# Kernel optimization log

Measured on AMD Instinct MI355X. Metric: run time of the kernel, lower is better.

## Reference

```python
import jax, jax.numpy as jnp
import numpy as np

N_E = 1024
E_DIM = 256
BETA = 0.25
PERSISTENCE = 0.1
B, T = 16, 1024


def setup_inputs() -> dict:
    key = jax.random.key(0)
    k1, k2 = jax.random.split(key)
    z = jax.random.normal(k1, (B, T, E_DIM), dtype=jnp.float32)
    # nn.Embedding(1+n_e, e_dim) init uniform(-1/n_e, 1/n_e)
    emb_weight = jax.random.uniform(k2, (N_E + 1, E_DIM), dtype=jnp.float32,
                                    minval=-1.0 / N_E, maxval=1.0 / N_E)
    return {"z": z, "emb_weight": emb_weight}


def _loss_contrast(z, ind, book):
    # z: (B,T,e), ind: (B,T) int, book: (n_e+1, e)
    z_q = book[ind]                                   # (B,T,e)
    loss_indices = jnp.sum((z - z_q) ** 2, axis=-1)   # (B,T)
    # ||z - book||^2 expanded to avoid the (B,T,n_e+1,e) intermediate
    z_sq = jnp.sum(z * z, axis=-1)                    # (B,T)
    b_sq = jnp.sum(book * book, axis=-1)              # (n_e+1,)
    cross = jnp.einsum('bte,ne->btn', z, book)        # (B,T,n_e+1)
    loss_all = z_sq[..., None] + b_sq[None, None, :] - 2.0 * cross
    lc = jnp.maximum(loss_indices[..., None] - loss_all + 1e-6 / N_E, 0.0)
    return jnp.mean(lc)


def _forward(z, emb_weight):
    zf = z.reshape(-1, E_DIM)
    d = (jnp.sum(zf * zf, axis=1, keepdims=True)
         + jnp.sum(emb_weight * emb_weight, axis=1)
         - 2.0 * (zf @ emb_weight.T)).reshape(B, T, N_E + 1)

    ind0 = jnp.clip(jnp.argmin(d[:, 0, :], axis=1), 0, N_E - 1)  # (B,)

    def step(carry, d_t):
        ind, coe = carry                              # (B,) int, (B,) f32
        d_here = jnp.take_along_axis(d_t, ind[:, None], axis=1)[:, 0]
        ind_next = jnp.minimum(ind + 1, N_E - 1)
        d_next = jnp.take_along_axis(d_t, ind_next[:, None], axis=1)[:, 0]
        stay = d_here <= d_next - coe
        ind_new = jnp.where(stay, ind, ind_next)
        coe_new = jnp.where(stay, coe + PERSISTENCE / N_E, 0.0)
        return (ind_new, coe_new), ind_new

    coe0 = jnp.zeros((B,), jnp.float32)
    _, inds = jax.lax.scan(step, (ind0, coe0), jnp.swapaxes(d[:, 1:, :], 0, 1))
    encoding_indices = jnp.concatenate([ind0[None, :], inds], axis=0).T  # (B,T)

    book_sg = jax.lax.stop_gradient(emb_weight)  # torch uses .data/.detach() everywhere
    z_q_raw = book_sg[encoding_indices]
    z_q = z + jax.lax.stop_gradient(z_q_raw - z)  # straight-through

    # non-legacy: beta * L(z, sg(book)) + L(sg(z), sg(book))
    loss = (BETA * _loss_contrast(z, encoding_indices, book_sg)
            + _loss_contrast(jax.lax.stop_gradient(z), encoding_indices, book_sg))

    v = jnp.max(encoding_indices) - jnp.min(encoding_indices)
    return z_q, loss, encoding_indices, v


def reference(z, emb_weight):
    return _forward(z, emb_weight)
```

## Files before the change

kernel.cpp:

```cpp
#include <hip/hip_runtime.h>

#define N_E   1024
#define EDIM  256
#define BB    16
#define TT    1024
#define NROW  (BB*TT)
#define NCOL  1025
#define NPAD  1152
#define PERS  (0.1f/1024.0f)
#define EPSC  (1e-6f/1024.0f)

#define OUT_LOSS 4194304
#define OUT_IDX  4194305
#define OUT_V    4210689

#define WS_ZB   0ull
#define WS_BBF  8388608ull
#define WS_BSQ  8978432ull
#define WS_E    8983552ull
#define WS_IND  84481024ull
#define WS_PART 84546560ull

typedef __attribute__((ext_vector_type(8))) short short8;
typedef __attribute__((ext_vector_type(4))) float floatx4;

__device__ __forceinline__ unsigned short f2bf(float f) {
    unsigned int u = __float_as_uint(f);
    u = (u + 0x7fffu + ((u >> 16) & 1u)) >> 16;
    return (unsigned short)u;
}

__global__ __launch_bounds__(256) void k0_prep(const float* __restrict__ z,
                                               const float* __restrict__ book,
                                               unsigned short* __restrict__ zb,
                                               unsigned short* __restrict__ bb,
                                               float* __restrict__ bsq) {
    int bx = blockIdx.x, tid = threadIdx.x;
    if (bx < 4096) {
        float4 v = ((const float4*)z)[bx * 256 + tid];
        size_t o = ((size_t)bx * 256 + tid) * 4;
        zb[o + 0] = f2bf(v.x); zb[o + 1] = f2bf(v.y);
        zb[o + 2] = f2bf(v.z); zb[o + 3] = f2bf(v.w);
    } else {
        int row = bx - 4096;
        float v = (row < NCOL) ? book[(size_t)row * EDIM + tid] : 0.0f;
        bb[(size_t)row * EDIM + tid] = f2bf(v);
        __shared__ float sd[256];
        sd[tid] = v * v;
        __syncthreads();
        for (int s = 128; s > 0; s >>= 1) { if (tid < s) sd[tid] += sd[tid + s]; __syncthreads(); }
        if (tid == 0) bsq[row] = sd[0];
    }
}

__global__ __launch_bounds__(256) void k1_gemm(const unsigned short* __restrict__ zb,
                                               const unsigned short* __restrict__ bb,
                                               const float* __restrict__ bsq,
                                               float* __restrict__ e) {
    int tid = threadIdx.x;
    int lane = tid & 63, w = tid >> 6;
    int mBase = blockIdx.x * 128 + (w >> 1) * 64;
    int nBase = blockIdx.y * 128 + (w & 1) * 64;
    int r = lane & 15, q = lane >> 4;

    floatx4 acc[4][4];
    #pragma unroll
    for (int i = 0; i < 4; i++)
        #pragma unroll
        for (int j = 0; j < 4; j++) acc[i][j] = (floatx4){0.f, 0.f, 0.f, 0.f};

    const short8* A = (const short8*)zb;
    const short8* Bm = (const short8*)bb;

    #pragma unroll
    for (int ks = 0; ks < 8; ks++) {
        int k8 = ks * 4 + q;
        short8 a[4], b[4];
        #pragma unroll
        for (int i = 0; i < 4; i++) a[i] = A[(size_t)(mBase + i * 16 + r) * 32 + k8];
        #pragma unroll
        for (int j = 0; j < 4; j++) b[j] = Bm[(size_t)(nBase + j * 16 + r) * 32 + k8];
        #pragma unroll
        for (int i = 0; i < 4; i++)
            #pragma unroll
            for (int j = 0; j < 4; j++)
                acc[i][j] = __builtin_amdgcn_mfma_f32_16x16x32_bf16(a[i], b[j], acc[i][j], 0, 0, 0);
    }

    float bsql[4];
    #pragma unroll
    for (int j = 0; j < 4; j++) bsql[j] = bsq[nBase + j * 16 + r];

    #pragma unroll
    for (int i = 0; i < 4; i++)
        #pragma unroll
        for (int rr = 0; rr < 4; rr++) {
            int m = mBase + i * 16 + q * 4 + rr;
            float* erow = e + (size_t)m * NPAD;
            #pragma unroll
            for (int j = 0; j < 4; j++)
                erow[nBase + j * 16 + r] = fmaf(-2.0f, acc[i][j][rr], bsql[j]);
        }
}

__global__ __launch_bounds__(256) void k2_scan(const float* __restrict__ z,
                                               const float* __restrict__ book,
                                               const float* __restrict__ bsq,
                                               const float* __restrict__ e,
                                               int* __restrict__ wind) {
    int b = blockIdx.x, tid = threadIdx.x;
    int lane = tid & 63, w = tid >> 6;

    const float4* zr = (const float4*)(z + (size_t)b * TT * EDIM);
    float4 zv = zr[lane];
    float s = zv.x * zv.x + zv.y * zv.y + zv.z * zv.z + zv.w * zv.w;
    #pragma unroll
    for (int off = 32; off; off >>= 1) s += __shfl_xor(s, off, 64);
    float zsq = s;

    float best = 3.4e38f; int bidx = 0;
    for (int wi = w; wi < 17; wi += 4) {
        int n = wi * 64 + lane;
        if (n < NCOL) {
            const float4* br = (const float4*)(book + (size_t)n * EDIM);
            float c0 = 0.f, c1 = 0.f, c2 = 0.f, c3 = 0.f;
            #pragma unroll 8
            for (int k = 0; k < 64; k++) {
                float4 bo = br[k]; float4 za = zr[k];
                c0 = fmaf(za.x, bo.x, c0); c1 = fmaf(za.y, bo.y, c1);
                c2 = fmaf(za.z, bo.z, c2); c3 = fmaf(za.w, bo.w, c3);
            }
            float cr = (c0 + c1) + (c2 + c3);
            float d0 = (zsq + bsq[n]) - 2.0f * cr;
            if (d0 < best || (d0 == best && n < bidx)) { best = d0; bidx = n; }
        }
    }
    #pragma unroll
    for (int off = 32; off; off >>= 1) {
        float ob = __shfl_xor(best, off, 64);
        int   oi = __shfl_xor(bidx, off, 64);
        if (ob < best || (ob == best && oi < bidx)) { best = ob; bidx = oi; }
    }
    __shared__ float sb[4]; __shared__ int si[4];
    if (lane == 0) { sb[w] = best; si[w] = bidx; }
    __syncthreads();
    if (w != 0) return;

    best = sb[0]; bidx = si[0];
    for (int i = 1; i < 4; i++) {
        float vv = sb[i]; int ii = si[i];
        if (vv < best || (vv == best && ii < bidx)) { best = vv; bidx = ii; }
    }

    int ind = min(bidx, N_E - 1);
    float coe = 0.0f;
    size_t ibase = (size_t)b * TT;
    if (lane == 0) wind[ibase] = ind;

    const float* eb = e + (size_t)b * TT * NPAD;
    float cur[30], nxt[30];
    int cb_cur = min(ind, 960);
    #pragma unroll
    for (int j = 0; j < 30; j++)
        cur[j] = eb[(size_t)(1 + j) * NPAD + cb_cur + lane];

    int t = 1;
    while (t < 1024) {
        int cb_nxt = min(ind, 960);
        #pragma unroll
        for (int j = 0; j < 30; j++) {
            int tn = t + 30 + j; tn = tn < 1024 ? tn : 1023;
            nxt[j] = eb[(size_t)tn * NPAD + cb_nxt + lane];
        }
        int packed = 0;
        #pragma unroll
        for (int j = 0; j < 30; j++) {
            if (t + j < 1024) {
                float here = __uint_as_float(__builtin_amdgcn_readlane(
                                 __float_as_uint(cur[j]), ind - cb_cur));
                int nc = min(ind + 1, N_E - 1);
                float nv = __uint_as_float(__builtin_amdgcn_readlane(
                                 __float_as_uint(cur[j]), nc - cb_cur));
                bool stay = (here <= nv - coe);
                ind = stay ? ind : nc;
                coe = stay ? (coe + PERS) : 0.0f;
                packed = (lane == j) ? ind : packed;
            }
        }
        if (lane < 30 && (t + lane) < 1024) wind[ibase + t + lane] = packed;
        #pragma unroll
        for (int j = 0; j < 30; j++) cur[j] = nxt[j];
        cb_cur = cb_nxt;
        t += 30;
    }
}

__global__ __launch_bounds__(256) void k3_loss_zq(const float* __restrict__ e,
                                                  const int* __restrict__ wind,
                                                  const float* __restrict__ book,
                                                  float* __restrict__ part,
                                                  float* __restrict__ out) {
    int rIdx = blockIdx.x, tid = threadIdx.x;
    int ind = wind[rIdx];
    const float* er = e + (size_t)rIdx * NPAD;
    float eind = er[ind];
    float p = 0.0f;
    for (int n = tid; n < NCOL; n += 256) {
        float v = eind - er[n] + EPSC;
        p += v > 0.0f ? v : 0.0f;
    }
    __shared__ float sd[256];
    sd[tid] = p; __syncthreads();
    for (int s = 128; s > 0; s >>= 1) { if (tid < s) sd[tid] += sd[tid + s]; __syncthreads(); }
    if (tid == 0) { part[rIdx] = sd[0]; out[OUT_IDX + rIdx] = (float)ind; }
    out[(size_t)rIdx * 256 + tid] = book[(size_t)ind * EDIM + tid];
}

__global__ __launch_bounds__(256) void k4_final(const float* __restrict__ part,
                                                const int* __restrict__ wind,
                                                float* __restrict__ out) {
    int tid = threadIdx.x;
    float s = 0.0f;
    for (int i = tid; i < NROW; i += 256) s += part[i];
    __shared__ float sd[256];
    sd[tid] = s; __syncthreads();
    for (int st = 128; st > 0; st >>= 1) { if (tid < st) sd[tid] += sd[tid + st]; __syncthreads(); }
    if (tid == 0) {
        int mn = wind[0], mx = wind[TT - 1];
        for (int b = 1; b < BB; b++) {
            mn = min(mn, wind[(size_t)b * TT]);
            mx = max(mx, wind[(size_t)b * TT + TT - 1]);
        }
        out[OUT_LOSS] = 1.25f * sd[0] / ((float)NROW * (float)NCOL);
        out[OUT_V] = (float)(mx - mn);
    }
}

extern "C" void kernel_launch(void* const* d_in, const int* in_sizes, int n_in,
                              void* d_out, int out_size, void* d_ws, size_t ws_size,
                              hipStream_t stream) {
    const float* z    = (const float*)d_in[0];
    const float* book = (const float*)d_in[1];
    char* ws = (char*)d_ws;
    unsigned short* zb = (unsigned short*)(ws + WS_ZB);
    unsigned short* bb = (unsigned short*)(ws + WS_BBF);
    float* bsq  = (float*)(ws + WS_BSQ);
    float* e    = (float*)(ws + WS_E);
    int*   wind = (int*)(ws + WS_IND);
    float* part = (float*)(ws + WS_PART);
    float* out  = (float*)d_out;

    hipLaunchKernelGGL(k0_prep,    dim3(4096 + 1152), dim3(256), 0, stream, z, book, zb, bb, bsq);
    hipLaunchKernelGGL(k1_gemm,    dim3(128, 9),      dim3(256), 0, stream, zb, bb, bsq, e);
    hipLaunchKernelGGL(k2_scan,    dim3(16),          dim3(256), 0, stream, z, book, bsq, e, wind);
    hipLaunchKernelGGL(k3_loss_zq, dim3(16384),       dim3(256), 0, stream, e, wind, book, part, out);
    hipLaunchKernelGGL(k4_final,   dim3(1),           dim3(256), 0, stream, part, wind, out);
}
```

Baseline: 263.0 us.

## Quantize scan stay-test into integer thresholds with one readlane per step

The sequential per-batch scan now precomputes, for each lane and time step, an integer threshold floor((d_next - d_here)/PERS). This turns the float comparison with the accumulating coe into an integer counter test, so each serial step needs one readlane instead of two and a shorter dependency chain. The chunk size grows from 30 to 31 steps so the loop covers exactly 1023 steps with no bounds checks. The quantization may not exactly match the float comparison in edge cases, since the reference accumulates coe as a float sum.

```diff
diff --git a/kernel.cpp b/kernel.cpp
--- a/kernel.cpp
+++ b/kernel.cpp
@@ -103,11 +103,11 @@
         }
 }
 
-__global__ __launch_bounds__(256) void k2_scan(const float* __restrict__ z,
-                                               const float* __restrict__ book,
-                                               const float* __restrict__ bsq,
-                                               const float* __restrict__ e,
-                                               int* __restrict__ wind) {
+__global__ __launch_bounds__(256, 1) void k2_scan(const float* __restrict__ z,
+                                                  const float* __restrict__ book,
+                                                  const float* __restrict__ bsq,
+                                                  const float* __restrict__ e,
+                                                  int* __restrict__ wind) {
     int b = blockIdx.x, tid = threadIdx.x;
     int lane = tid & 63, w = tid >> 6;
 
@@ -153,45 +153,64 @@
     }
 
     int ind = min(bidx, N_E - 1);
-    float coe = 0.0f;
+    int kk = 0;
     size_t ibase = (size_t)b * TT;
     if (lane == 0) wind[ibase] = ind;
 
     const float* eb = e + (size_t)b * TT * NPAD;
-    float cur[30], nxt[30];
-    int cb_cur = min(ind, 960);
-    #pragma unroll
-    for (int j = 0; j < 30; j++)
-        cur[j] = eb[(size_t)(1 + j) * NPAD + cb_cur + lane];
+    const float QS = 1.0f / PERS;
+
+    float Av[31], Bv[31];
+    int   q[31];
+
+    int cb = min(ind, 960);
+    {
+        #pragma unroll
+        for (int j = 0; j < 31; j++) {
+            const float* p = eb + (size_t)(1 + j) * NPAD + cb + lane;
+            Av[j] = p[0]; Bv[j] = p[1];
+        }
+        bool cap = (cb + lane == 1023);
+        #pragma unroll
+        for (int j = 0; j < 31; j++) {
+            int qv = (int)((Bv[j] - Av[j]) * QS);
+            q[j] = cap ? 0 : qv;
+        }
+    }
 
     int t = 1;
-    while (t < 1024) {
-        int cb_nxt = min(ind, 960);
-        #pragma unroll
-        for (int j = 0; j < 30; j++) {
-            int tn = t + 30 + j; tn = tn < 1024 ? tn : 1023;
-            nxt[j] = eb[(size_t)tn * NPAD + cb_nxt + lane];
+    for (int c = 0; c < 33; c++) {
+        int cbn = min(ind, 960);
+        if (c < 32) {
+            #pragma unroll
+            for (int j = 0; j < 31; j++) {
+                int tn = t + 31 + j; tn = tn < 1024 ? tn : 1023;
+                const float* p = eb + (size_t)tn * NPAD + cbn + lane;
+                Av[j] = p[0]; Bv[j] = p[1];
+            }
         }
         int packed = 0;
         #pragma unroll
-        for (int j = 0; j < 30; j++) {
-            if (t + j < 1024) {
-                float here = __uint_as_float(__builtin_amdgcn_readlane(
-                                 __float_as_uint(cur[j]), ind - cb_cur));
-                int nc = min(ind + 1, N_E - 1);
-                float nv = __uint_as_float(__builtin_amdgcn_readlane(
-                                 __float_as_uint(cur[j]), nc - cb_cur));
-                bool stay = (here <= nv - coe);
-                ind = stay ? ind : nc;
-                coe = stay ? (coe + PERS) : 0.0f;
-                packed = (lane == j) ? ind : packed;
+        for (int j = 0; j < 31; j++) {
+            int rel = ind - cb;
+            int qv = __builtin_amdgcn_readlane(q[j], rel);
+            bool stay = (kk <= qv);
+            int ip1 = ind + 1; ip1 = ip1 < 1023 ? ip1 : 1023;
+            ind = stay ? ind : ip1;
+            kk  = stay ? kk + 1 : 0;
+            packed = (lane == j) ? ind : packed;
+        }
+        if (lane < 31) wind[ibase + t + lane] = packed;
+        if (c < 32) {
+            bool cap = (cbn + lane == 1023);
+            #pragma unroll
+            for (int j = 0; j < 31; j++) {
+                int qv = (int)((Bv[j] - Av[j]) * QS);
+                q[j] = cap ? 0 : qv;
             }
         }
-        if (lane < 30 && (t + lane) < 1024) wind[ibase + t + lane] = packed;
-        #pragma unroll
-        for (int j = 0; j < 30; j++) cur[j] = nxt[j];
-        cb_cur = cb_nxt;
-        t += 30;
+        cb = cbn;
+        t += 31;
     }
 }
 
```

After: 260.3 us. No clear change (-1.0%).
